# Optimization experiments

Measured on AMD Instinct MI355X. Metric: run time of the kernel, lower is better.

## Reference

```python
import jax, jax.numpy as jnp
import numpy as np

N_KNOTS = 16
DEGREE = 3
EPS = 1e-8


def make_knots(n_knots, degree):
    knots = np.zeros(n_knots, dtype=np.float32)
    for i in range(n_knots):
        if i <= degree:
            knots[i] = 0.0
        elif i >= n_knots - degree - 1:
            knots[i] = 1.0
        else:
            knots[i] = (i - degree) / (n_knots - 2 * degree - 1)
    return knots


def setup_inputs() -> dict:
    key = jax.random.key(0)
    k1, k2 = jax.random.split(key)
    x = jax.random.uniform(k1, (65536, 64), dtype=jnp.float32)
    control_points = jax.random.normal(k2, (64, 12, 64), dtype=jnp.float32)
    return {"x": x, "control_points": control_points}


def bspline_basis(x, knots_np, degree):
    # x: [B, D] in [0,1]; returns basis: [B, D, n_control_points]
    n_knots = knots_np.shape[0]
    n_intervals = n_knots - 1
    knots = jnp.asarray(knots_np)
    xe = x[..., None]  # [B, D, 1]
    left = knots[:-1]
    right = knots[1:]
    in_interval = (xe >= left) & (xe < right)
    last = (xe >= left[-1]) & (xe <= right[-1])  # include right endpoint of last interval
    basis = jnp.concatenate([in_interval[..., :-1], last], axis=-1).astype(x.dtype)
    for k in range(1, degree + 1):
        nb = n_intervals - k
        j = np.arange(nb)
        dL = knots_np[j + k] - knots_np[j]          # constants
        dR = knots_np[j + k + 1] - knots_np[j + 1]
        okL = np.abs(dL) > EPS
        okR = np.abs(dR) > EPS
        invL = jnp.asarray(np.where(okL, 1.0 / np.where(okL, dL, 1.0), 0.0).astype(np.float32))
        invR = jnp.asarray(np.where(okR, 1.0 / np.where(okR, dR, 1.0), 0.0).astype(np.float32))
        cL = (xe - knots[j]) * invL                 # [B, D, nb], zero where degenerate
        cR = (knots[j + k + 1] - xe) * invR
        basis = cL * basis[..., :nb] + cR * basis[..., 1:nb + 1]
    return basis


def reference(x, control_points):
    # x: [B, in_dim]; control_points: [in_dim, n_cp, out_dim]
    knots_np = make_knots(N_KNOTS, DEGREE)
    xc = jnp.clip(x, 0.0, 1.0)
    basis = bspline_basis(xc, knots_np, DEGREE)     # [B, in_dim, n_cp]
    return jnp.einsum('bic,ico->bo', basis, control_points)
```

## Files before the change

kernel.cpp:

```cpp
#include <hip/hip_runtime.h>


typedef short short8 __attribute__((ext_vector_type(8)));
typedef float f32x4 __attribute__((ext_vector_type(4)));

#define NFEAT 64
#define KTOT  768
#define NSTEP 24
#define CHUNK 32
#define CHUNKS 4
#define RPB   (CHUNK*CHUNKS)
#define THREADS 256
#define LPAD  776

static __device__ __forceinline__ unsigned bf16rne(float f) {
  unsigned u = __float_as_uint(f);
  return (u + 0x7FFFu + ((u >> 16) & 1u)) >> 16;
}

__global__ __launch_bounds__(256) void prep_wfrag(const float* __restrict__ cp,
                                                  unsigned* __restrict__ wfrag) {
  int id = blockIdx.x * 256 + threadIdx.x;
  int d  = id & 3;
  int l  = (id >> 2) & 63;
  int id2 = id >> 8;
  int nt = id2 / NSTEP;
  int s  = id2 - nt * NSTEP;
  int g  = l >> 4;
  int o  = nt * 16 + (l & 15);
  int e0 = 2 * d;
  int k0 = s * 32 + ((e0 < 4) ? (4 * g + e0) : (16 + 4 * g + (e0 - 4)));
  int k1 = k0 + 1;
  unsigned lo = bf16rne(cp[k0 * 64 + o]);
  unsigned hi = bf16rne(cp[k1 * 64 + o]);
  wfrag[id] = lo | (hi << 16);
}

__global__ __launch_bounds__(THREADS) void kan_mfma(const float* __restrict__ x,
                                                    const unsigned* __restrict__ wfrag,
                                                    float* __restrict__ out) {
  __shared__ short bs[CHUNK * LPAD];
  const int tid  = threadIdx.x;
  const int lane = tid & 63;
  const int w    = tid >> 6;
  const long rowBase = (long)blockIdx.x * RPB;

  short8 bfr[NSTEP];
  {
    const short8* wp = (const short8*)wfrag + (w * NSTEP * 64 + lane);
    #pragma unroll
    for (int s = 0; s < NSTEP; ++s) bfr[s] = wp[s * 64];
  }

  const int r  = tid & (CHUNK - 1);
  const int fg = tid >> 5;

  for (int c = 0; c < CHUNKS; ++c) {
    const float* xrow = x + (rowBase + c * CHUNK + r) * 64 + fg * 8;
    float4 xv0 = ((const float4*)xrow)[0];
    float4 xv1 = ((const float4*)xrow)[1];
    float xs8[8] = {xv0.x, xv0.y, xv0.z, xv0.w, xv1.x, xv1.y, xv1.z, xv1.w};

    #pragma unroll
    for (int e = 0; e < 8; ++e) {
      float xi = fminf(fmaxf(xs8[e], 0.0f), 1.0f);
      float t9 = xi * 9.0f;
      int jj = (int)t9;
      float validf = (jj <= 8) ? 1.0f : 0.0f;
      jj = (jj > 8) ? 8 : jj;
      float fj = (float)jj;
      float u  = t9 - fj;
      float omu = 1.0f - u;
      float c1  = fminf(fj, 1.0f);
      float c2  = fminf(fj, 2.0f);
      float rdj = 9.0f - fj;
      float d2p = fminf(rdj, 2.0f);
      float d3p = fminf(rdj, 3.0f);
      float invA = (jj == 0) ? 1.0f : 0.5f;
      float invB = (jj == 8) ? 1.0f : 0.5f;
      float invC = (jj == 0) ? 1.0f : ((jj == 1) ? 0.5f : (1.0f/3.0f));
      float invD = (jj == 0 || jj == 8) ? 0.5f : (1.0f/3.0f);
      float invE = (jj >= 7) ? ((jj == 8) ? 1.0f : 0.5f) : (1.0f/3.0f);
      float xkm1 = u + c1, xkm2 = u + c2;
      float k2x = d2p - u, k3x = d3p - u;
      float t0 = omu * invA;
      float A0 = omu * t0;
      float s1 = xkm1 * t0;
      float t1 = u * invB;
      float A1 = fmaf(k2x, t1, s1);
      float A2 = u * t1;
      float u0 = A0 * invC;
      float B0 = omu * u0;
      float s2 = xkm2 * u0;
      float u1 = A1 * invD;
      float B1 = fmaf(k2x, u1, s2);
      float s3 = xkm1 * u1;
      float u2 = A2 * invE;
      float B2 = fmaf(k3x, u2, s3);
      float B3 = u * u2;
      B0 *= validf; B1 *= validf; B2 *= validf; B3 *= validf;

      unsigned b0 = bf16rne(B0), b1 = bf16rne(B1), b2 = bf16rne(B2), b3 = bf16rne(B3);
      unsigned p01 = b0 | (b1 << 16);
      unsigned p23 = b2 | (b3 << 16);
      unsigned O0 = p01 << 16;
      unsigned O1 = (p01 >> 16) | (p23 << 16);
      unsigned O2 = p23 >> 16;
      int e2 = jj >> 1;
      bool odd = (jj & 1) != 0;
      unsigned wd[6];
      #pragma unroll
      for (int q = 0; q < 6; ++q) {
        unsigned ve = (q == e2) ? p01 : ((q == e2 + 1) ? p23 : 0u);
        unsigned vo = (q == e2) ? O0 : ((q == e2 + 1) ? O1 : ((q == e2 + 2) ? O2 : 0u));
        wd[q] = odd ? vo : ve;
      }
      uint2* dst = (uint2*)(bs + (r * LPAD + (fg * 8 + e) * 12));
      dst[0] = make_uint2(wd[0], wd[1]);
      dst[1] = make_uint2(wd[2], wd[3]);
      dst[2] = make_uint2(wd[4], wd[5]);
    }

    __syncthreads();

    #pragma unroll
    for (int rt = 0; rt < 2; ++rt) {
      f32x4 acc = {0.0f, 0.0f, 0.0f, 0.0f};
      const short* ap = bs + (rt * 16 + (lane & 15)) * LPAD + (lane >> 4) * 4;
      #pragma unroll
      for (int s = 0; s < NSTEP; ++s) {
        union { struct { uint2 a, b; } p; short8 v; } fa;
        fa.p.a = *(const uint2*)(ap + s * 32);
        fa.p.b = *(const uint2*)(ap + s * 32 + 16);
        acc = __builtin_amdgcn_mfma_f32_16x16x32_bf16(fa.v, bfr[s], acc, 0, 0, 0);
      }
      const long orow = rowBase + c * CHUNK + rt * 16 + (lane >> 4) * 4;
      const int  ocol = w * 16 + (lane & 15);
      #pragma unroll
      for (int j = 0; j < 4; ++j)
        out[(orow + j) * 64 + ocol] = acc[j];
    }

    __syncthreads();
  }
}

extern "C" void kernel_launch(void* const* d_in, const int* in_sizes, int n_in,
                              void* d_out, int out_size, void* d_ws, size_t ws_size,
                              hipStream_t stream) {
  const float* x  = (const float*)d_in[0];
  const float* cp = (const float*)d_in[1];
  float* out = (float*)d_out;
  unsigned* wfrag = (unsigned*)d_ws;

  hipLaunchKernelGGL(prep_wfrag, dim3(96), dim3(256), 0, stream, cp, wfrag);
  const int rows = in_sizes[0] / NFEAT;
  hipLaunchKernelGGL(kan_mfma, dim3(rows / RPB), dim3(THREADS), 0, stream,
                     x, wfrag, out);
}
```

Measured before the change: 88.48 us.

## Double-buffer basis tiles in LDS and overlap evaluation with MFMA

The shared basis buffer is split into two halves of 16 rows each. The next chunk's x is prefetched and its basis evaluated into the spare buffer while the MFMA loop consumes the current one, which leaves one barrier per chunk instead of two. The LDS row stride changes to an odd dword count (387) to spread bank access, and each thread now evaluates 4 features instead of 8. Risks are smaller MFMA batches per sync and 32-bit scalar LDS reads that may be less vectorized.

```diff
diff --git a/kernel.cpp b/kernel.cpp
--- a/kernel.cpp
+++ b/kernel.cpp
@@ -3,15 +3,15 @@
 
 typedef short short8 __attribute__((ext_vector_type(8)));
 typedef float f32x4 __attribute__((ext_vector_type(4)));
+typedef unsigned u32x4 __attribute__((ext_vector_type(4)));
 
 #define NFEAT 64
-#define KTOT  768
 #define NSTEP 24
-#define CHUNK 32
-#define CHUNKS 4
+#define CHUNK 16
+#define CHUNKS 8
 #define RPB   (CHUNK*CHUNKS)
 #define THREADS 256
-#define LPAD  776
+#define RDW   387
 
 static __device__ __forceinline__ unsigned bf16rne(float f) {
   unsigned u = __float_as_uint(f);
@@ -30,16 +30,69 @@
   int o  = nt * 16 + (l & 15);
   int e0 = 2 * d;
   int k0 = s * 32 + ((e0 < 4) ? (4 * g + e0) : (16 + 4 * g + (e0 - 4)));
-  int k1 = k0 + 1;
   unsigned lo = bf16rne(cp[k0 * 64 + o]);
-  unsigned hi = bf16rne(cp[k1 * 64 + o]);
+  unsigned hi = bf16rne(cp[(k0 + 1) * 64 + o]);
   wfrag[id] = lo | (hi << 16);
+}
+
+static __device__ __forceinline__ void eval_pack(float xi, unsigned* __restrict__ dst) {
+  xi = fminf(fmaxf(xi, 0.0f), 1.0f);
+  float t9 = xi * 9.0f;
+  int jj = (int)t9;
+  float validf = (jj <= 8) ? 1.0f : 0.0f;
+  jj = (jj > 8) ? 8 : jj;
+  float fj = (float)jj;
+  float u  = t9 - fj;
+  float omu = 1.0f - u;
+  float c1  = fminf(fj, 1.0f);
+  float c2  = fminf(fj, 2.0f);
+  float rdj = 9.0f - fj;
+  float d2p = fminf(rdj, 2.0f);
+  float d3p = fminf(rdj, 3.0f);
+  float invA = (jj == 0) ? 1.0f : 0.5f;
+  float invB = (jj == 8) ? 1.0f : 0.5f;
+  float invC = (jj == 0) ? 1.0f : ((jj == 1) ? 0.5f : (1.0f/3.0f));
+  float invD = (jj == 0 || jj == 8) ? 0.5f : (1.0f/3.0f);
+  float invE = (jj >= 7) ? ((jj == 8) ? 1.0f : 0.5f) : (1.0f/3.0f);
+  float xkm1 = u + c1, xkm2 = u + c2;
+  float k2x = d2p - u, k3x = d3p - u;
+  float t0 = omu * invA;
+  float A0 = omu * t0;
+  float s1 = xkm1 * t0;
+  float t1 = u * invB;
+  float A1 = fmaf(k2x, t1, s1);
+  float A2 = u * t1;
+  float u0 = A0 * invC;
+  float B0 = omu * u0;
+  float s2 = xkm2 * u0;
+  float u1 = A1 * invD;
+  float B1 = fmaf(k2x, u1, s2);
+  float s3 = xkm1 * u1;
+  float u2 = A2 * invE;
+  float B2 = fmaf(k3x, u2, s3);
+  float B3 = u * u2;
+  B0 *= validf; B1 *= validf; B2 *= validf; B3 *= validf;
+
+  unsigned b0 = bf16rne(B0), b1 = bf16rne(B1), b2 = bf16rne(B2), b3 = bf16rne(B3);
+  unsigned p01 = b0 | (b1 << 16);
+  unsigned p23 = b2 | (b3 << 16);
+  unsigned O0 = p01 << 16;
+  unsigned O1 = (p01 >> 16) | (p23 << 16);
+  unsigned O2 = p23 >> 16;
+  int e2 = jj >> 1;
+  bool odd = (jj & 1) != 0;
+  #pragma unroll
+  for (int q = 0; q < 6; ++q) {
+    unsigned ve = (q == e2) ? p01 : ((q == e2 + 1) ? p23 : 0u);
+    unsigned vo = (q == e2) ? O0 : ((q == e2 + 1) ? O1 : ((q == e2 + 2) ? O2 : 0u));
+    dst[q] = odd ? vo : ve;
+  }
 }
 
 __global__ __launch_bounds__(THREADS) void kan_mfma(const float* __restrict__ x,
                                                     const unsigned* __restrict__ wfrag,
                                                     float* __restrict__ out) {
-  __shared__ short bs[CHUNK * LPAD];
+  __shared__ unsigned bsd[2][CHUNK * RDW];
   const int tid  = threadIdx.x;
   const int lane = tid & 63;
   const int w    = tid >> 6;
@@ -52,95 +105,51 @@
     for (int s = 0; s < NSTEP; ++s) bfr[s] = wp[s * 64];
   }
 
-  const int r  = tid & (CHUNK - 1);
-  const int fg = tid >> 5;
+  const int br  = tid >> 4;
+  const int bi0 = (tid & 15) * 4;
+  const int m = lane & 15, g = lane >> 4;
+
+  {
+    const float4 xv = *(const float4*)(x + (rowBase + br) * 64 + bi0);
+    float xs4[4] = {xv.x, xv.y, xv.z, xv.w};
+    #pragma unroll
+    for (int e = 0; e < 4; ++e)
+      eval_pack(xs4[e], &bsd[0][br * RDW + (bi0 + e) * 6]);
+  }
+  __syncthreads();
 
   for (int c = 0; c < CHUNKS; ++c) {
-    const float* xrow = x + (rowBase + c * CHUNK + r) * 64 + fg * 8;
-    float4 xv0 = ((const float4*)xrow)[0];
-    float4 xv1 = ((const float4*)xrow)[1];
-    float xs8[8] = {xv0.x, xv0.y, xv0.z, xv0.w, xv1.x, xv1.y, xv1.z, xv1.w};
+    const int cur = c & 1;
 
-    #pragma unroll
-    for (int e = 0; e < 8; ++e) {
-      float xi = fminf(fmaxf(xs8[e], 0.0f), 1.0f);
-      float t9 = xi * 9.0f;
-      int jj = (int)t9;
-      float validf = (jj <= 8) ? 1.0f : 0.0f;
-      jj = (jj > 8) ? 8 : jj;
-      float fj = (float)jj;
-      float u  = t9 - fj;
-      float omu = 1.0f - u;
-      float c1  = fminf(fj, 1.0f);
-      float c2  = fminf(fj, 2.0f);
-      float rdj = 9.0f - fj;
-      float d2p = fminf(rdj, 2.0f);
-      float d3p = fminf(rdj, 3.0f);
-      float invA = (jj == 0) ? 1.0f : 0.5f;
-      float invB = (jj == 8) ? 1.0f : 0.5f;
-      float invC = (jj == 0) ? 1.0f : ((jj == 1) ? 0.5f : (1.0f/3.0f));
-      float invD = (jj == 0 || jj == 8) ? 0.5f : (1.0f/3.0f);
-      float invE = (jj >= 7) ? ((jj == 8) ? 1.0f : 0.5f) : (1.0f/3.0f);
-      float xkm1 = u + c1, xkm2 = u + c2;
-      float k2x = d2p - u, k3x = d3p - u;
-      float t0 = omu * invA;
-      float A0 = omu * t0;
-      float s1 = xkm1 * t0;
-      float t1 = u * invB;
-      float A1 = fmaf(k2x, t1, s1);
-      float A2 = u * t1;
-      float u0 = A0 * invC;
-      float B0 = omu * u0;
-      float s2 = xkm2 * u0;
-      float u1 = A1 * invD;
-      float B1 = fmaf(k2x, u1, s2);
-      float s3 = xkm1 * u1;
-      float u2 = A2 * invE;
-      float B2 = fmaf(k3x, u2, s3);
-      float B3 = u * u2;
-      B0 *= validf; B1 *= validf; B2 *= validf; B3 *= validf;
-
-      unsigned b0 = bf16rne(B0), b1 = bf16rne(B1), b2 = bf16rne(B2), b3 = bf16rne(B3);
-      unsigned p01 = b0 | (b1 << 16);
-      unsigned p23 = b2 | (b3 << 16);
-      unsigned O0 = p01 << 16;
-      unsigned O1 = (p01 >> 16) | (p23 << 16);
-      unsigned O2 = p23 >> 16;
-      int e2 = jj >> 1;
-      bool odd = (jj & 1) != 0;
-      unsigned wd[6];
-      #pragma unroll
-      for (int q = 0; q < 6; ++q) {
-        unsigned ve = (q == e2) ? p01 : ((q == e2 + 1) ? p23 : 0u);
-        unsigned vo = (q == e2) ? O0 : ((q == e2 + 1) ? O1 : ((q == e2 + 2) ? O2 : 0u));
-        wd[q] = odd ? vo : ve;
-      }
-      uint2* dst = (uint2*)(bs + (r * LPAD + (fg * 8 + e) * 12));
-      dst[0] = make_uint2(wd[0], wd[1]);
-      dst[1] = make_uint2(wd[2], wd[3]);
-      dst[2] = make_uint2(wd[4], wd[5]);
+    float xs4[4];
+    if (c < CHUNKS - 1) {
+      const float4 xv = *(const float4*)(x + (rowBase + (c + 1) * CHUNK + br) * 64 + bi0);
+      xs4[0] = xv.x; xs4[1] = xv.y; xs4[2] = xv.z; xs4[3] = xv.w;
     }
 
-    __syncthreads();
-
-    #pragma unroll
-    for (int rt = 0; rt < 2; ++rt) {
-      f32x4 acc = {0.0f, 0.0f, 0.0f, 0.0f};
-      const short* ap = bs + (rt * 16 + (lane & 15)) * LPAD + (lane >> 4) * 4;
+    f32x4 acc = {0.0f, 0.0f, 0.0f, 0.0f};
+    {
+      const short* base = (const short*)&bsd[cur][0] + m * (2 * RDW) + g * 4;
       #pragma unroll
       for (int s = 0; s < NSTEP; ++s) {
-        union { struct { uint2 a, b; } p; short8 v; } fa;
-        fa.p.a = *(const uint2*)(ap + s * 32);
-        fa.p.b = *(const uint2*)(ap + s * 32 + 16);
-        acc = __builtin_amdgcn_mfma_f32_16x16x32_bf16(fa.v, bfr[s], acc, 0, 0, 0);
+        const unsigned* pa = (const unsigned*)(base + s * 32);
+        const unsigned* pb = (const unsigned*)(base + s * 32 + 16);
+        u32x4 q = { pa[0], pa[1], pb[0], pb[1] };
+        acc = __builtin_amdgcn_mfma_f32_16x16x32_bf16(
+            __builtin_bit_cast(short8, q), bfr[s], acc, 0, 0, 0);
       }
-      const long orow = rowBase + c * CHUNK + rt * 16 + (lane >> 4) * 4;
-      const int  ocol = w * 16 + (lane & 15);
+    }
+    {
+      float* op = out + (rowBase + c * CHUNK + g * 4) * 64 + w * 16 + m;
       #pragma unroll
-      for (int j = 0; j < 4; ++j)
-        out[(orow + j) * 64 + ocol] = acc[j];
+      for (int j = 0; j < 4; ++j) op[j * 64] = acc[j];
     }
 
+    if (c < CHUNKS - 1) {
+      #pragma unroll
+      for (int e = 0; e < 4; ++e)
+        eval_pack(xs4[e], &bsd[cur ^ 1][br * RDW + (bi0 + e) * 6]);
+    }
     __syncthreads();
   }
 }
```

New measurement: 90.61 us. +2.4%, slower.
